# Kernel optimization log

Measured on AMD Instinct MI355X. Metric: run time of the kernel, lower is better.

The kernel has to match this reference:

```python
import jax, jax.numpy as jnp
import numpy as np

B, S, D = 4, 2048, 1024
H, DK, DV = 16, 64, 64

def setup_inputs() -> dict:
    key = jax.random.key(0)
    ks = jax.random.split(key, 8)
    def xavier(k, fan_in, fan_out):
        limit = float(np.sqrt(6.0 / (fan_in + fan_out)))
        return jax.random.uniform(k, (fan_in, fan_out), jnp.float32, -limit, limit)
    return {
        "Q": jax.random.normal(ks[0], (B, S, D), jnp.float32),
        "K": jax.random.normal(ks[1], (B, S, D), jnp.float32),
        "V": jax.random.normal(ks[2], (B, S, D), jnp.float32),
        "mask": jax.random.uniform(ks[3], (B, S), jnp.float32),
        "Wq": xavier(ks[4], D, H * DK),  # stored [in, out]; torch Linear applies x @ W.T
        "bq": jnp.zeros((H * DK,), jnp.float32),
        "Wk": xavier(ks[5], D, H * DK),
        "bk": jnp.zeros((H * DK,), jnp.float32),
        "Wv": xavier(ks[6], D, H * DV),
        "bv": jnp.zeros((H * DV,), jnp.float32),
    }

def reference(Q, K, V, mask, Wq, bq, Wk, bk, Wv, bv):
    b, s, _ = Q.shape
    # projections -> [b, h, s, d]
    q = (Q @ Wq + bq).reshape(b, s, H, DK).transpose(0, 2, 1, 3)
    k = (K @ Wk + bk).reshape(b, s, H, DK).transpose(0, 2, 1, 3)
    v = (V @ Wv + bv).reshape(b, s, H, DV).transpose(0, 2, 1, 3)
    scores = jnp.einsum('bhqd,bhkd->bhqk', q, k) / jnp.sqrt(jnp.float32(DK))
    e = jnp.exp(scores)  # NOTE: raw exp, no max-subtraction (faithful to source)
    e = e * mask[:, None, None, :]  # multiplicative mask over key dim
    attn = e / (jnp.sum(e, axis=-1, keepdims=True) + 1e-8)
    context = jnp.einsum('bhqk,bhkd->bhqd', attn, v)
    return context.transpose(0, 2, 1, 3).reshape(b, s, H * DV)
```

## Files before the change

### kernel.cpp

```cpp
#include <hip/hip_runtime.h>
#include <hip/hip_bf16.h>
#include <stdint.h>

typedef short bf16x8 __attribute__((ext_vector_type(8)));
typedef float f32x4 __attribute__((ext_vector_type(4)));
typedef unsigned int u32x2 __attribute__((ext_vector_type(2)));
typedef unsigned int u32x4 __attribute__((ext_vector_type(4)));

__device__ __forceinline__ unsigned short f2bf(float f) {
  union { float f; unsigned u; } x; x.f = f;
  unsigned r = x.u + 0x7FFFu + ((x.u >> 16) & 1u);
  return (unsigned short)(r >> 16);
}

__device__ __forceinline__ unsigned pk2bf(float a, float b) {
  union { __hip_bfloat162 h; unsigned u; } x;
  x.h = __float22bfloat162_rn(make_float2(a, b));
  return x.u;
}

__device__ __forceinline__ float exp2_fast(float x) {
#if __has_builtin(__builtin_amdgcn_exp2f)
  return __builtin_amdgcn_exp2f(x);
#else
  float r; asm("v_exp_f32 %0, %1" : "=v"(r) : "v"(x)); return r;
#endif
}

typedef const __attribute__((address_space(1))) unsigned int* gptr_t;
typedef __attribute__((address_space(3))) unsigned int* lptr_t;
__device__ __forceinline__ void gll16(const void* g, void* l) {
  __builtin_amdgcn_global_load_lds((gptr_t)g, (lptr_t)l, 16, 0, 0);
}

#define QSCALE 0.18033688011116f

__global__ __launch_bounds__(1024) void wt_kernel(const float* __restrict__ Wq,
                                                  const float* __restrict__ Wk,
                                                  const float* __restrict__ Wv,
                                                  unsigned short* __restrict__ wt) {
  const float* W = blockIdx.z == 0 ? Wq : (blockIdx.z == 1 ? Wk : Wv);
  unsigned short* o = wt + (size_t)blockIdx.z * 1048576;
  __shared__ float t[32][33];
  int tx = threadIdx.x, ty = threadIdx.y;
  t[ty][tx] = W[(size_t)(blockIdx.y * 32 + ty) * 1024 + blockIdx.x * 32 + tx];
  __syncthreads();
  o[(size_t)(blockIdx.x * 32 + ty) * 1024 + blockIdx.y * 32 + tx] = f2bf(t[tx][ty]);
}

__global__ __launch_bounds__(256) void cvt_kernel(const float* __restrict__ Q,
                                                  const float* __restrict__ K,
                                                  const float* __restrict__ V,
                                                  unsigned short* __restrict__ out) {
  int y = blockIdx.y;
  const float* s = y == 0 ? Q : (y == 1 ? K : V);
  unsigned short* o = out + (size_t)y * 8388608;
  size_t idx = ((size_t)blockIdx.x * 256 + threadIdx.x) * 8;
  float4 f0 = *(const float4*)(s + idx);
  float4 f1 = *(const float4*)(s + idx + 4);
  u32x4 r = {pk2bf(f0.x, f0.y), pk2bf(f0.z, f0.w), pk2bf(f1.x, f1.y), pk2bf(f1.z, f1.w)};
  *(u32x4*)(o + idx) = r;
}

__global__ __launch_bounds__(256, 3) void proj_kernel(
    const unsigned short* __restrict__ Xb, const unsigned short* __restrict__ wt,
    const float* __restrict__ bq, const float* __restrict__ bk, const float* __restrict__ bv,
    const float* __restrict__ mask,
    unsigned short* __restrict__ qo, unsigned short* __restrict__ ko, unsigned short* __restrict__ vo) {
  int p = blockIdx.z;
  const unsigned short* X = Xb + (size_t)p * 8388608;
  const unsigned short* Wt = wt + (size_t)p * 1048576;
  const float* bias = p == 0 ? bq : (p == 1 ? bk : bv);
  unsigned short* out = p == 0 ? qo : (p == 1 ? ko : vo);

  __shared__ __align__(16) unsigned short sbuf[3][8192];

  int tid = threadIdx.x;
  int lane = tid & 63, w = tid >> 6;
  int l15 = lane & 15, quad = lane >> 4;
  int wm = w >> 1, wn = w & 1;
  int m0 = blockIdx.x * 128, n0 = blockIdx.y * 128;

  const unsigned short* src[4];
  unsigned dstoff[4];
#pragma unroll
  for (int j = 0; j < 4; ++j) {
    int stj = w * 4 + j;
    if (stj < 8) src[j] = Wt + (size_t)(n0 + stj * 16 + l15) * 1024 + quad * 8;
    else         src[j] = X  + (size_t)(m0 + (stj - 8) * 16 + l15) * 1024 + quad * 8;
    dstoff[j] = stj * 512;
  }

  f32x4 acc[4][4] = {};

#define PSTAGE(sb, t)                                           \
  do {                                                          \
    _Pragma("unroll")                                           \
    for (int j = 0; j < 4; ++j)                                 \
      gll16(src[j] + (size_t)(t) * 32, &sbuf[sb][dstoff[j]]);   \
  } while (0)

#define PCOMPUTE(cb)                                                          \
  do {                                                                        \
    bf16x8 af[4], bfr[4];                                                     \
    _Pragma("unroll")                                                         \
    for (int i = 0; i < 4; ++i)                                               \
      af[i] = *(const bf16x8*)&sbuf[cb][4096 + (wm * 4 + i) * 512 + lane * 8];\
    _Pragma("unroll")                                                         \
    for (int j = 0; j < 4; ++j)                                               \
      bfr[j] = *(const bf16x8*)&sbuf[cb][(wn * 4 + j) * 512 + lane * 8];      \
    _Pragma("unroll")                                                         \
    for (int i = 0; i < 4; ++i)                                               \
      _Pragma("unroll")                                                       \
      for (int j = 0; j < 4; ++j)                                             \
        acc[i][j] = __builtin_amdgcn_mfma_f32_16x16x32_bf16(af[i], bfr[j], acc[i][j], 0, 0, 0); \
  } while (0)

#define PSYNC(n)                                                    \
  do {                                                              \
    asm volatile("s_waitcnt vmcnt(" #n ") lgkmcnt(0)" ::: "memory");\
    __builtin_amdgcn_sched_barrier(0);                              \
    __builtin_amdgcn_s_barrier();                                   \
    __builtin_amdgcn_sched_barrier(0);                              \
  } while (0)

  PSTAGE(0, 0);
  PSTAGE(1, 1);
  PSYNC(4);

  for (int g = 0; g < 10; ++g) {
    int t = g * 3;
    PSTAGE(2, t + 2);  PCOMPUTE(0);  PSYNC(4);
    PSTAGE(0, t + 3);  PCOMPUTE(1);  PSYNC(4);
    PSTAGE(1, t + 4);  PCOMPUTE(2);  PSYNC(4);
  }
  PCOMPUTE(0);
  PSYNC(0);
  PCOMPUTE(1);

#undef PSTAGE
#undef PCOMPUTE
#undef PSYNC

  __syncthreads();

  unsigned short* cl = &sbuf[0][0];
  bool isv = (p == 2);
  bool isq = (p == 0);

  for (int j = 0; j < 4; ++j) {
    int n = wn * 64 + j * 16 + l15;
    float bl = bias[n0 + n];
    for (int i = 0; i < 4; ++i) {
      int mb = wm * 64 + i * 16 + quad * 4;
      if (isv) {
        union { unsigned short s4[4]; u32x2 v; } pk;
        for (int r = 0; r < 4; ++r) {
          float val = acc[i][j][r] + bl;
          val *= mask[m0 + mb + r];
          pk.s4[r] = f2bf(val);
        }
        *(u32x2*)&cl[n * 136 + mb] = pk.v;
      } else {
        for (int r = 0; r < 4; ++r) {
          float val = acc[i][j][r] + bl;
          if (isq) val *= QSCALE;
          cl[(mb + r) * 136 + n] = f2bf(val);
        }
      }
    }
  }
  __syncthreads();

  int b = m0 >> 11;
  int sloc = m0 & 2047;
  int ch = tid & 7;
  for (int pass = 0; pass < 8; ++pass) {
    int rr = pass * 32 + (tid >> 3);
    int row = rr >> 1, half = rr & 1;
    const unsigned short* sr = &cl[row * 136 + half * 64 + ch * 8];
    unsigned short* dst;
    if (isv) {
      int nn = n0 + row;
      int h = nn >> 6, d = nn & 63;
      dst = out + (((size_t)((b * 16 + h) * 64 + d)) << 11) + sloc + half * 64 + ch * 8;
    } else {
      int s = sloc + row;
      int h = (n0 >> 6) + half;
      dst = out + (((size_t)((b * 16 + h) * 2048 + s)) << 6) + ch * 8;
    }
    *(u32x4*)dst = *(const u32x4*)sr;
  }
}

__global__ __launch_bounds__(512, 4) void attn_kernel(
    const unsigned short* __restrict__ q, const unsigned short* __restrict__ k,
    const unsigned short* __restrict__ vT, const float* __restrict__ mask,
    float* __restrict__ out) {
  int qb = blockIdx.x, h = blockIdx.y, b = blockIdx.z;
  int tid = threadIdx.x, lane = tid & 63, w = tid >> 6;
  int l15 = lane & 15, quad = lane >> 4;

  __shared__ __align__(16) unsigned short kbuf[2][4096];
  __shared__ __align__(16) unsigned short vbuf[2][4096];
  __shared__ __align__(16) unsigned short pbuf[8][2048];

  const unsigned short* qp = q + (size_t)(b * 16 + h) * 2048 * 64;
  const unsigned short* kp = k + (size_t)(b * 16 + h) * 2048 * 64;
  const unsigned short* vp = vT + (size_t)(b * 16 + h) * 64 * 2048;
  const float* mp = mask + (size_t)b * 2048;

  bf16x8 aq[2][2];
  for (int nt = 0; nt < 2; ++nt)
    for (int kt = 0; kt < 2; ++kt)
      aq[nt][kt] = *(const bf16x8*)(qp + (size_t)(qb * 256 + w * 32 + nt * 16 + l15) * 64 + kt * 32 + quad * 8);

  f32x4 oacc[2][4] = {};
  f32x4 dacc[2] = {};

  unsigned short* pw = pbuf[w];

  int skt = w >> 2, sm = w & 3;
  const unsigned short* ksrc0 = kp + (size_t)(sm * 16 + l15) * 64 + skt * 32 + quad * 8;
  const unsigned short* vsrc0 = vp + (size_t)(sm * 16 + l15) * 2048 + skt * 32 + quad * 8;

#define STAGE(bi, t)                                    \
  do {                                                  \
    gll16(ksrc0 + (size_t)(t) * 64 * 64, &kbuf[bi][w * 512]); \
    gll16(vsrc0 + (size_t)(t) * 64,      &vbuf[bi][w * 512]); \
  } while (0)

  STAGE(0, 0);
  __syncthreads();

  for (int t = 0; t < 32; ++t) {
    int cur = t & 1;
    if (t + 1 < 32) STAGE(cur ^ 1, t + 1);

    f32x4 sacc[4][2] = {};
    __builtin_amdgcn_s_setprio(1);
    for (int m = 0; m < 4; ++m)
      for (int kt = 0; kt < 2; ++kt) {
        bf16x8 ak = *(const bf16x8*)&kbuf[cur][(kt * 4 + m) * 512 + lane * 8];
        sacc[m][0] = __builtin_amdgcn_mfma_f32_16x16x32_bf16(ak, aq[0][kt], sacc[m][0], 0, 0, 0);
        sacc[m][1] = __builtin_amdgcn_mfma_f32_16x16x32_bf16(ak, aq[1][kt], sacc[m][1], 0, 0, 0);
      }
    __builtin_amdgcn_s_setprio(0);

    for (int m = 0; m < 4; ++m)
      for (int nt = 0; nt < 2; ++nt) {
        float e0 = exp2_fast(sacc[m][nt][0]);
        float e1 = exp2_fast(sacc[m][nt][1]);
        float e2 = exp2_fast(sacc[m][nt][2]);
        float e3 = exp2_fast(sacc[m][nt][3]);
        u32x2 wv = {pk2bf(e0, e1), pk2bf(e2, e3)};
        *(u32x2*)&pw[(nt * 4 + m) * 256 + lane * 4] = wv;
      }

    int kbase = t * 64;
    for (int kt = 0; kt < 2; ++kt) {
      int m = kt * 2 + (quad >> 1);
      int srcl = ((quad & 1) * 2) * 16 + l15;
      bf16x8 pa[2];
      for (int mt = 0; mt < 2; ++mt) {
        union { u32x2 p[2]; bf16x8 v; } u;
        int base = (mt * 4 + m) * 256 + srcl * 4;
        u.p[0] = *(const u32x2*)&pw[base];
        u.p[1] = *(const u32x2*)&pw[base + 64];
        pa[mt] = u.v;
      }
      float4 m0v = *(const float4*)&mp[kbase + kt * 32 + quad * 8];
      float4 m1v = *(const float4*)&mp[kbase + kt * 32 + quad * 8 + 4];
      union { u32x4 u; bf16x8 v; } mu;
      mu.u = (u32x4){pk2bf(m0v.x, m0v.y), pk2bf(m0v.z, m0v.w),
                     pk2bf(m1v.x, m1v.y), pk2bf(m1v.z, m1v.w)};
      __builtin_amdgcn_s_setprio(1);
      dacc[0] = __builtin_amdgcn_mfma_f32_16x16x32_bf16(pa[0], mu.v, dacc[0], 0, 0, 0);
      dacc[1] = __builtin_amdgcn_mfma_f32_16x16x32_bf16(pa[1], mu.v, dacc[1], 0, 0, 0);
      for (int nt = 0; nt < 4; ++nt) {
        bf16x8 bv = *(const bf16x8*)&vbuf[cur][(kt * 4 + nt) * 512 + lane * 8];
        oacc[0][nt] = __builtin_amdgcn_mfma_f32_16x16x32_bf16(pa[0], bv, oacc[0][nt], 0, 0, 0);
        oacc[1][nt] = __builtin_amdgcn_mfma_f32_16x16x32_bf16(pa[1], bv, oacc[1][nt], 0, 0, 0);
      }
      __builtin_amdgcn_s_setprio(0);
    }
    __syncthreads();
  }
#undef STAGE

  for (int mt = 0; mt < 2; ++mt)
    for (int r = 0; r < 4; ++r) {
      int s = qb * 256 + w * 32 + mt * 16 + quad * 4 + r;
      float rden = 1.0f / (dacc[mt][r] + 1e-8f);
      for (int nt = 0; nt < 4; ++nt) {
        int dv = nt * 16 + l15;
        out[(size_t)(b * 2048 + s) * 1024 + h * 64 + dv] = oacc[mt][nt][r] * rden;
      }
    }
}

extern "C" void kernel_launch(void* const* d_in, const int* in_sizes, int n_in,
                              void* d_out, int out_size, void* d_ws, size_t ws_size,
                              hipStream_t stream) {
  const float* Q    = (const float*)d_in[0];
  const float* K    = (const float*)d_in[1];
  const float* V    = (const float*)d_in[2];
  const float* mask = (const float*)d_in[3];
  const float* Wq   = (const float*)d_in[4];
  const float* bq   = (const float*)d_in[5];
  const float* Wk   = (const float*)d_in[6];
  const float* bk   = (const float*)d_in[7];
  const float* Wv   = (const float*)d_in[8];
  const float* bv   = (const float*)d_in[9];

  char* ws = (char*)d_ws;
  unsigned short* wt = (unsigned short*)ws;
  unsigned short* qb = (unsigned short*)(ws + 6291456);
  unsigned short* kb = (unsigned short*)(ws + 23068672);
  unsigned short* vb = (unsigned short*)(ws + 39845888);
  unsigned short* xb = (unsigned short*)(ws + 56623104);

  hipLaunchKernelGGL(wt_kernel, dim3(32, 32, 3), dim3(32, 32), 0, stream, Wq, Wk, Wv, wt);
  hipLaunchKernelGGL(cvt_kernel, dim3(4096, 3), dim3(256), 0, stream, Q, K, V, xb);
  hipLaunchKernelGGL(proj_kernel, dim3(64, 8, 3), dim3(256), 0, stream,
                     xb, wt, bq, bk, bv, mask, qb, kb, vb);
  hipLaunchKernelGGL(attn_kernel, dim3(8, 16, 4), dim3(512), 0, stream,
                     qb, kb, vb, mask, (float*)d_out);
}
```

Baseline: 353.4 us.

## Halve P buffer, stage mask in LDS as bf16, raise occupancy hint

```diff
diff --git a/kernel.cpp b/kernel.cpp
--- a/kernel.cpp
+++ b/kernel.cpp
@@ -193,7 +193,7 @@
   }
 }
 
-__global__ __launch_bounds__(512, 4) void attn_kernel(
+__global__ __launch_bounds__(512, 6) void attn_kernel(
     const unsigned short* __restrict__ q, const unsigned short* __restrict__ k,
     const unsigned short* __restrict__ vT, const float* __restrict__ mask,
     float* __restrict__ out) {
@@ -203,7 +203,8 @@
 
   __shared__ __align__(16) unsigned short kbuf[2][4096];
   __shared__ __align__(16) unsigned short vbuf[2][4096];
-  __shared__ __align__(16) unsigned short pbuf[8][2048];
+  __shared__ __align__(16) unsigned short pbuf[8][1024];
+  __shared__ __align__(16) unsigned short mlds[2048];
 
   const unsigned short* qp = q + (size_t)(b * 16 + h) * 2048 * 64;
   const unsigned short* kp = k + (size_t)(b * 16 + h) * 2048 * 64;
@@ -230,6 +231,12 @@
     gll16(vsrc0 + (size_t)(t) * 64,      &vbuf[bi][w * 512]); \
   } while (0)
 
+  {
+    int t4 = tid * 4;
+    float4 mv4 = *(const float4*)&mp[t4];
+    u32x2 mw = {pk2bf(mv4.x, mv4.y), pk2bf(mv4.z, mv4.w)};
+    *(u32x2*)&mlds[t4] = mw;
+  }
   STAGE(0, 0);
   __syncthreads();
 
@@ -247,36 +254,40 @@
       }
     __builtin_amdgcn_s_setprio(0);
 
-    for (int m = 0; m < 4; ++m)
-      for (int nt = 0; nt < 2; ++nt) {
-        float e0 = exp2_fast(sacc[m][nt][0]);
-        float e1 = exp2_fast(sacc[m][nt][1]);
-        float e2 = exp2_fast(sacc[m][nt][2]);
-        float e3 = exp2_fast(sacc[m][nt][3]);
-        u32x2 wv = {pk2bf(e0, e1), pk2bf(e2, e3)};
-        *(u32x2*)&pw[(nt * 4 + m) * 256 + lane * 4] = wv;
-      }
-
     int kbase = t * 64;
+#pragma unroll
     for (int kt = 0; kt < 2; ++kt) {
-      int m = kt * 2 + (quad >> 1);
+#pragma unroll
+      for (int mloc = 0; mloc < 2; ++mloc) {
+        int m = kt * 2 + mloc;
+#pragma unroll
+        for (int nt = 0; nt < 2; ++nt) {
+          float e0 = exp2_fast(sacc[m][nt][0]);
+          float e1 = exp2_fast(sacc[m][nt][1]);
+          float e2 = exp2_fast(sacc[m][nt][2]);
+          float e3 = exp2_fast(sacc[m][nt][3]);
+          u32x2 wv = {pk2bf(e0, e1), pk2bf(e2, e3)};
+          *(u32x2*)&pw[(nt * 2 + mloc) * 256 + lane * 4] = wv;
+        }
+      }
+
+      int mloc_src = quad >> 1;
       int srcl = ((quad & 1) * 2) * 16 + l15;
       bf16x8 pa[2];
+#pragma unroll
       for (int mt = 0; mt < 2; ++mt) {
         union { u32x2 p[2]; bf16x8 v; } u;
-        int base = (mt * 4 + m) * 256 + srcl * 4;
+        int base = (mt * 2 + mloc_src) * 256 + srcl * 4;
         u.p[0] = *(const u32x2*)&pw[base];
         u.p[1] = *(const u32x2*)&pw[base + 64];
         pa[mt] = u.v;
       }
-      float4 m0v = *(const float4*)&mp[kbase + kt * 32 + quad * 8];
-      float4 m1v = *(const float4*)&mp[kbase + kt * 32 + quad * 8 + 4];
-      union { u32x4 u; bf16x8 v; } mu;
-      mu.u = (u32x4){pk2bf(m0v.x, m0v.y), pk2bf(m0v.z, m0v.w),
-                     pk2bf(m1v.x, m1v.y), pk2bf(m1v.z, m1v.w)};
+      bf16x8 mv = *(const bf16x8*)&mlds[kbase + kt * 32 + quad * 8];
+
       __builtin_amdgcn_s_setprio(1);
-      dacc[0] = __builtin_amdgcn_mfma_f32_16x16x32_bf16(pa[0], mu.v, dacc[0], 0, 0, 0);
-      dacc[1] = __builtin_amdgcn_mfma_f32_16x16x32_bf16(pa[1], mu.v, dacc[1], 0, 0, 0);
+      dacc[0] = __builtin_amdgcn_mfma_f32_16x16x32_bf16(pa[0], mv, dacc[0], 0, 0, 0);
+      dacc[1] = __builtin_amdgcn_mfma_f32_16x16x32_bf16(pa[1], mv, dacc[1], 0, 0, 0);
+#pragma unroll
       for (int nt = 0; nt < 4; ++nt) {
         bf16x8 bv = *(const bf16x8*)&vbuf[cur][(kt * 4 + nt) * 512 + lane * 8];
         oacc[0][nt] = __builtin_amdgcn_mfma_f32_16x16x32_bf16(pa[0], bv, oacc[0][nt], 0, 0, 0);
```

Measured after the change: 655.0 us. +85.4%, slower.
